# Performance work log

Hardware: AMD Instinct MI355X
Metric: run time of the kernel (lower is better)

## Reference

```python
import jax, jax.numpy as jnp
import numpy as np

L_SPAN = 8          # max event span length
MAX_ITER = 3        # args.max_iteration + 1
RATE = 0.3          # confidence threshold for edge creation
BETA_INTRA = 0.7
BETA_INTER = 0.3


def setup_inputs() -> dict:
    key = jax.random.key(0)
    ks = jax.random.split(key, 16)
    n_sents, S, D = 64, 512, 768
    E, P, NL, H, C = 2000, 20000, 128, 512, 3
    sc = lambda fan: 1.0 / np.sqrt(fan)
    return {
        'sent_emb': jax.random.normal(ks[0], (n_sents, S, D), jnp.float32),
        'W_proj': jax.random.normal(ks[1], (D, NL), jnp.float32) * sc(D),
        'W1': jax.random.normal(ks[2], (2 * D + NL, H), jnp.float32) * sc(2 * D + NL),
        'b1': jnp.zeros((H,), jnp.float32),
        'W2': jax.random.normal(ks[3], (H, C), jnp.float32) * sc(H),
        'b2': jnp.zeros((C,), jnp.float32),
        'W_self': jax.random.normal(ks[4], (NL, NL), jnp.float32) * sc(NL),
        'W_intra': jax.random.normal(ks[5], (NL, NL), jnp.float32) * sc(NL),
        'W_inter': jax.random.normal(ks[6], (NL, NL), jnp.float32) * sc(NL),
        'event_sent': jax.random.randint(ks[7], (E,), 0, n_sents, jnp.int32),
        'event_start': jax.random.randint(ks[8], (E,), 0, S - L_SPAN, jnp.int32),
        'event_len': jax.random.randint(ks[9], (E,), 0, L_SPAN, jnp.int32),
        'pair1': jax.random.randint(ks[10], (P,), 0, E, jnp.int32),
        'pair2': jax.random.randint(ks[11], (P,), 0, E, jnp.int32),
        'rel_type': jax.random.randint(ks[12], (P,), 0, 2, jnp.int32),
        'target': jax.random.randint(ks[13], (P,), 0, 3, jnp.int32),
    }


def _extract_events(sent_emb, event_sent, event_start, event_len):
    # ragged span mean: spans have length 1..L_SPAN
    S = sent_emb.shape[1]
    lens = (event_len + 1).astype(sent_emb.dtype)            # [E]
    offs = jnp.arange(L_SPAN)
    idx = jnp.clip(event_start[:, None] + offs[None, :], 0, S - 1)  # [E, L]
    tok = sent_emb[event_sent[:, None], idx]                 # [E, L, D] gather
    mask = (offs[None, :] < (event_len + 1)[:, None]).astype(sent_emb.dtype)
    return (tok * mask[:, :, None]).sum(1) / lens[:, None]   # [E, D]


def reference(sent_emb, W_proj, W1, b1, W2, b2, W_self, W_intra, W_inter,
              event_sent, event_start, event_len, pair1, pair2, rel_type, target):
    E = event_sent.shape[0]
    e_emb = _extract_events(sent_emb, event_sent, event_start, event_len)   # [E, 768]
    event_pair_embed = jnp.concatenate([e_emb[pair1], e_emb[pair2]], axis=-1)  # [P, 1536]
    x = e_emb @ W_proj                                                      # [E, n_last]

    seg = jax.ops.segment_sum
    loss = jnp.float32(0.0)
    logits = None
    for it in range(MAX_ITER):
        diff = x[pair1] - x[pair2]                                          # [P, n_last]
        feats = jnp.concatenate([event_pair_embed, diff], axis=-1)          # [P, 1536+n_last]
        logits = jax.nn.relu(feats @ W1 + b1) @ W2 + b2                     # [P, C]
        logp = jax.nn.log_softmax(logits, axis=-1)
        ce = -jnp.take_along_axis(logp, target[:, None], axis=-1).mean()
        loss = loss + ce / (it + 1)

        # dynamic graph construction from predictions
        p = jax.nn.softmax(logits, axis=-1)
        conf = p.max(-1) > RATE
        argm = p.argmax(-1)
        f = lambda m: jax.lax.stop_gradient(m.astype(x.dtype))[:, None]
        mi1 = f(conf & (argm == 1) & (rel_type == 0))   # intra: pair1 -> pair2
        mi2 = f(conf & (argm == 2) & (rel_type == 0))   # intra reversed
        me1 = f(conf & (argm == 1) & (rel_type == 1))   # inter
        me2 = f(conf & (argm == 2) & (rel_type == 1))

        # intra aggregation (includes self-loop)
        s_intra = seg(x[pair1] * mi1, pair2, num_segments=E) + \
                  seg(x[pair2] * mi2, pair1, num_segments=E) + x
        c_intra = seg(mi1[:, 0], pair2, num_segments=E) + \
                  seg(mi2[:, 0], pair1, num_segments=E) + 1.0
        agg_intra = s_intra / c_intra[:, None]

        s_inter = seg(x[pair1] * me1, pair2, num_segments=E) + \
                  seg(x[pair2] * me2, pair1, num_segments=E)
        c_inter = seg(me1[:, 0], pair2, num_segments=E) + \
                  seg(me2[:, 0], pair1, num_segments=E)
        agg_inter = s_inter / jnp.maximum(c_inter, 1.0)[:, None]

        x = jax.nn.relu(x @ W_self + BETA_INTRA * (agg_intra @ W_intra)
                        + BETA_INTER * (agg_inter @ W_inter))
    return loss, logits
```

## Files before the change

kernel.cpp:

```cpp
#include <hip/hip_runtime.h>
#include <hip/hip_bf16.h>


#define D_DIM 768
#define H_DIM 512
#define NL_DIM 128

__global__ __launch_bounds__(256) void extract_kernel(
    const float* __restrict__ sent_emb, const int* __restrict__ es,
    const int* __restrict__ st, const int* __restrict__ el,
    float* __restrict__ e_emb)
{
    int e = blockIdx.x;
    int t = threadIdx.x;
    int s = es[e];
    int start = st[e];
    int len = el[e] + 1;
    const float* base = sent_emb + ((size_t)s * 512 + start) * D_DIM;
    float a0 = 0.f, a1 = 0.f, a2 = 0.f;
    for (int k = 0; k < len; ++k) {
        const float* row = base + (size_t)k * D_DIM;
        a0 += row[t];
        a1 += row[t + 256];
        a2 += row[t + 512];
    }
    float inv = 1.0f / (float)len;
    float* out = e_emb + (size_t)e * D_DIM;
    out[t]       = a0 * inv;
    out[t + 256] = a1 * inv;
    out[t + 512] = a2 * inv;
}

#define GBM 64
#define GBN 64
#define GBK 16
__global__ __launch_bounds__(256) void gemm_f32(
    const float* __restrict__ A, int lda,
    const float* __restrict__ B, int ldb,
    float* __restrict__ C, int ldc,
    int M, int N, int K, int flags)
{
    __shared__ float As[GBK][GBM + 4];
    __shared__ float Bs[GBK][GBN];
    int t = threadIdx.x;
    int m0 = blockIdx.y * GBM;
    int n0 = blockIdx.x * GBN;
    int tm = t >> 4;
    int tn = t & 15;
    int arow = t >> 2;
    int akc  = (t & 3) * 4;
    int bkr  = t >> 4;
    int bnc  = (t & 15) * 4;

    float acc[4][4];
#pragma unroll
    for (int i = 0; i < 4; ++i)
#pragma unroll
        for (int j = 0; j < 4; ++j) acc[i][j] = 0.f;

    for (int k0 = 0; k0 < K; k0 += GBK) {
        float4 av = make_float4(0.f, 0.f, 0.f, 0.f);
        if (m0 + arow < M)
            av = *(const float4*)(A + (size_t)(m0 + arow) * lda + k0 + akc);
        As[akc + 0][arow] = av.x;
        As[akc + 1][arow] = av.y;
        As[akc + 2][arow] = av.z;
        As[akc + 3][arow] = av.w;
        float4 bv = *(const float4*)(B + (size_t)(k0 + bkr) * ldb + n0 + bnc);
        *(float4*)&Bs[bkr][bnc] = bv;
        __syncthreads();
#pragma unroll
        for (int k = 0; k < GBK; ++k) {
            float4 a = *(const float4*)&As[k][tm * 4];
            float4 b = *(const float4*)&Bs[k][tn * 4];
            acc[0][0] += a.x * b.x; acc[0][1] += a.x * b.y; acc[0][2] += a.x * b.z; acc[0][3] += a.x * b.w;
            acc[1][0] += a.y * b.x; acc[1][1] += a.y * b.y; acc[1][2] += a.y * b.z; acc[1][3] += a.y * b.w;
            acc[2][0] += a.z * b.x; acc[2][1] += a.z * b.y; acc[2][2] += a.z * b.z; acc[2][3] += a.z * b.w;
            acc[3][0] += a.w * b.x; acc[3][1] += a.w * b.y; acc[3][2] += a.w * b.z; acc[3][3] += a.w * b.w;
        }
        __syncthreads();
    }
#pragma unroll
    for (int i = 0; i < 4; ++i) {
        int row = m0 + tm * 4 + i;
        if (row < M) {
            float* cp = C + (size_t)row * ldc + n0 + tn * 4;
#pragma unroll
            for (int j = 0; j < 4; ++j) {
                float v = acc[i][j];
                if (flags & 1) v += cp[j];
                if (flags & 2) v = fmaxf(v, 0.f);
                cp[j] = v;
            }
        }
    }
}

__global__ __launch_bounds__(256) void zero4_kernel(float4* __restrict__ p, int n4)
{
    int i = blockIdx.x * 256 + threadIdx.x;
    if (i < n4) p[i] = make_float4(0.f, 0.f, 0.f, 0.f);
}

__global__ __launch_bounds__(256) void pair_kernel(
    const float* __restrict__ A1, const float* __restrict__ A2,
    const float* __restrict__ Y, const float* __restrict__ X,
    const float* __restrict__ b1, const float* __restrict__ W2,
    const float* __restrict__ b2,
    const int* __restrict__ pair1, const int* __restrict__ pair2,
    const int* __restrict__ rel, const int* __restrict__ tgt,
    float* s_intra, float* s_inter, float* c_intra, float* c_inter,
    float* __restrict__ ce_out, float* logits_out, int P, int do_scatter)
{
    __shared__ float ce_sh[4];
    int t = threadIdx.x;
    int wave = t >> 6;
    int lane = t & 63;
    int p = blockIdx.x * 4 + wave;
    float ce = 0.f;
    if (p < P) {
        int p1 = pair1[p], p2 = pair2[p];
        int base = lane * 8;
        float a1f[8], a2f[8], y1f[8], y2f[8], b1f[8], w2f[24];
        {
            const float4* a1p = (const float4*)(A1 + (size_t)p1 * H_DIM + base);
            const float4* a2p = (const float4*)(A2 + (size_t)p2 * H_DIM + base);
            const float4* y1p = (const float4*)(Y + (size_t)p1 * H_DIM + base);
            const float4* y2p = (const float4*)(Y + (size_t)p2 * H_DIM + base);
            const float4* b1p = (const float4*)(b1 + base);
            const float4* w2p = (const float4*)(W2 + (size_t)base * 3);
            *(float4*)&a1f[0] = a1p[0]; *(float4*)&a1f[4] = a1p[1];
            *(float4*)&a2f[0] = a2p[0]; *(float4*)&a2f[4] = a2p[1];
            *(float4*)&y1f[0] = y1p[0]; *(float4*)&y1f[4] = y1p[1];
            *(float4*)&y2f[0] = y2p[0]; *(float4*)&y2f[4] = y2p[1];
            *(float4*)&b1f[0] = b1p[0]; *(float4*)&b1f[4] = b1p[1];
#pragma unroll
            for (int q = 0; q < 6; ++q) *(float4*)&w2f[q * 4] = w2p[q];
        }
        float l0 = 0.f, l1 = 0.f, l2 = 0.f;
#pragma unroll
        for (int i = 0; i < 8; ++i) {
            float h = a1f[i] + a2f[i] + y1f[i] - y2f[i] + b1f[i];
            h = fmaxf(h, 0.f);
            l0 += h * w2f[i * 3 + 0];
            l1 += h * w2f[i * 3 + 1];
            l2 += h * w2f[i * 3 + 2];
        }
#pragma unroll
        for (int off = 32; off > 0; off >>= 1) {
            l0 += __shfl_xor(l0, off);
            l1 += __shfl_xor(l1, off);
            l2 += __shfl_xor(l2, off);
        }
        l0 += b2[0]; l1 += b2[1]; l2 += b2[2];
        float m = fmaxf(l0, fmaxf(l1, l2));
        float lse = m + logf(expf(l0 - m) + expf(l1 - m) + expf(l2 - m));
        int tg = tgt[p];
        float lt = (tg == 0) ? l0 : ((tg == 1) ? l1 : l2);
        ce = lse - lt;
        if (logits_out && lane == 0) {
            logits_out[(size_t)p * 3 + 0] = l0;
            logits_out[(size_t)p * 3 + 1] = l1;
            logits_out[(size_t)p * 3 + 2] = l2;
        }
        if (do_scatter) {
            int argm = 0; float mx = l0;
            if (l1 > mx) { mx = l1; argm = 1; }
            if (l2 > mx) { mx = l2; argm = 2; }
            if (argm != 0) {
                int r = rel[p];
                int src = (argm == 1) ? p1 : p2;
                int dst = (argm == 1) ? p2 : p1;
                float* sacc = (r == 0) ? s_intra : s_inter;
                float* cacc = (r == 0) ? c_intra : c_inter;
                const float* xs = X + (size_t)src * NL_DIM;
                float* sd = sacc + (size_t)dst * NL_DIM;
                atomicAdd(&sd[lane], xs[lane]);
                atomicAdd(&sd[lane + 64], xs[lane + 64]);
                if (lane == 0) atomicAdd(&cacc[dst], 1.0f);
            }
        }
    }
    if (lane == 0) ce_sh[wave] = ce;
    __syncthreads();
    if (t == 0) ce_out[blockIdx.x] = ce_sh[0] + ce_sh[1] + ce_sh[2] + ce_sh[3];
}

__global__ __launch_bounds__(256) void agg_kernel(
    const float* __restrict__ s_intra, const float* __restrict__ s_inter,
    const float* __restrict__ c_intra, const float* __restrict__ c_inter,
    const float* __restrict__ X,
    float* __restrict__ aggI, float* __restrict__ aggE, int n)
{
    int i = blockIdx.x * 256 + threadIdx.x;
    if (i >= n) return;
    int e = i >> 7;
    float ci = c_intra[e] + 1.0f;
    float cf = fmaxf(c_inter[e], 1.0f);
    aggI[i] = 0.7f * (s_intra[i] + X[i]) / ci;
    aggE[i] = 0.3f * s_inter[i] / cf;
}

__global__ __launch_bounds__(256) void loss_kernel(
    const float* __restrict__ ce, int nblk, int P, float* __restrict__ out)
{
    int t = threadIdx.x;
    float acc = 0.f;
    for (int it = 0; it < 3; ++it) {
        float w = 1.0f / ((float)P * (float)(it + 1));
        for (int i = t; i < nblk; i += 256)
            acc += ce[(size_t)it * nblk + i] * w;
    }
    __shared__ float red[256];
    red[t] = acc;
    __syncthreads();
    for (int s = 128; s > 0; s >>= 1) {
        if (t < s) red[t] += red[t + s];
        __syncthreads();
    }
    if (t == 0) out[0] = red[0];
}

extern "C" void kernel_launch(void* const* d_in, const int* in_sizes, int n_in,
                              void* d_out, int out_size, void* d_ws, size_t ws_size,
                              hipStream_t stream)
{
    const float* sent_emb  = (const float*)d_in[0];
    const float* W_proj    = (const float*)d_in[1];
    const float* W1        = (const float*)d_in[2];
    const float* b1        = (const float*)d_in[3];
    const float* W2        = (const float*)d_in[4];
    const float* b2        = (const float*)d_in[5];
    const float* W_self    = (const float*)d_in[6];
    const float* W_intra   = (const float*)d_in[7];
    const float* W_inter   = (const float*)d_in[8];
    const int* event_sent  = (const int*)d_in[9];
    const int* event_start = (const int*)d_in[10];
    const int* event_len   = (const int*)d_in[11];
    const int* pair1       = (const int*)d_in[12];
    const int* pair2       = (const int*)d_in[13];
    const int* rel_type    = (const int*)d_in[14];
    const int* target      = (const int*)d_in[15];

    int E = in_sizes[9];
    int P = in_sizes[12];
    float* out = (float*)d_out;
    float* ws  = (float*)d_ws;

    size_t o = 0;
    float* e_emb   = ws + o; o += (size_t)E * D_DIM;
    float* A1      = ws + o; o += (size_t)E * H_DIM;
    float* A2      = ws + o; o += (size_t)E * H_DIM;
    float* Yb      = ws + o; o += (size_t)E * H_DIM;
    float* X0      = ws + o; o += (size_t)E * NL_DIM;
    float* X1      = ws + o; o += (size_t)E * NL_DIM;
    float* s_intra = ws + o; o += (size_t)E * NL_DIM;
    float* s_inter = ws + o; o += (size_t)E * NL_DIM;
    float* c_intra = ws + o; o += (size_t)E;
    float* c_inter = ws + o; o += (size_t)E;
    float* aggI    = ws + o; o += (size_t)E * NL_DIM;
    float* aggE    = ws + o; o += (size_t)E * NL_DIM;
    int NBLK = (P + 3) / 4;
    float* ceb     = ws + o; o += (size_t)3 * NBLK;

    extract_kernel<<<E, 256, 0, stream>>>(sent_emb, event_sent, event_start, event_len, e_emb);

    dim3 gA(H_DIM / GBN, (E + GBM - 1) / GBM);
    dim3 gX(NL_DIM / GBN, (E + GBM - 1) / GBM);
    gemm_f32<<<gA, 256, 0, stream>>>(e_emb, D_DIM, W1, H_DIM, A1, H_DIM, E, H_DIM, D_DIM, 0);
    gemm_f32<<<gA, 256, 0, stream>>>(e_emb, D_DIM, W1 + (size_t)D_DIM * H_DIM, H_DIM, A2, H_DIM, E, H_DIM, D_DIM, 0);
    gemm_f32<<<gX, 256, 0, stream>>>(e_emb, D_DIM, W_proj, NL_DIM, X0, NL_DIM, E, NL_DIM, D_DIM, 0);

    float* xcur = X0;
    float* xnext = X1;
    int zn4 = (E * NL_DIM * 2 + E * 2) / 4;
    for (int it = 0; it < 3; ++it) {
        int last = (it == 2);
        gemm_f32<<<gA, 256, 0, stream>>>(xcur, NL_DIM, W1 + (size_t)2 * D_DIM * H_DIM, H_DIM,
                                         Yb, H_DIM, E, H_DIM, NL_DIM, 0);
        if (!last)
            zero4_kernel<<<(zn4 + 255) / 256, 256, 0, stream>>>((float4*)s_intra, zn4);
        pair_kernel<<<NBLK, 256, 0, stream>>>(A1, A2, Yb, xcur, b1, W2, b2,
                                              pair1, pair2, rel_type, target,
                                              s_intra, s_inter, c_intra, c_inter,
                                              ceb + (size_t)it * NBLK,
                                              last ? (out + 1) : nullptr, P, !last);
        if (!last) {
            agg_kernel<<<(E * NL_DIM + 255) / 256, 256, 0, stream>>>(
                s_intra, s_inter, c_intra, c_inter, xcur, aggI, aggE, E * NL_DIM);
            gemm_f32<<<gX, 256, 0, stream>>>(xcur, NL_DIM, W_self, NL_DIM, xnext, NL_DIM, E, NL_DIM, NL_DIM, 0);
            gemm_f32<<<gX, 256, 0, stream>>>(aggI, NL_DIM, W_intra, NL_DIM, xnext, NL_DIM, E, NL_DIM, NL_DIM, 1);
            gemm_f32<<<gX, 256, 0, stream>>>(aggE, NL_DIM, W_inter, NL_DIM, xnext, NL_DIM, E, NL_DIM, NL_DIM, 1 | 2);
            float* tmp = xcur; xcur = xnext; xnext = tmp;
        }
    }
    loss_kernel<<<1, 256, 0, stream>>>(ceb, NBLK, P, out);
}
```

Baseline: 519.9 us.

## Fold A1/A2/b1 into GEMM epilogue and fuse GEMM launches

The Y GEMM epilogue now builds U = A1 + Y + b1 and V = A2 - Y per event, so the pair kernel gathers two 512-wide rows per pair instead of four and skips the b1 load. The three initial projections become one grid-partitioned launch, and the three update GEMMs become one kernel that accumulates all three products in registers and applies ReLU, with no read-modify-write of the output. The pair kernel handles four pairs per wave with W2 and b2 hoisted out of the pair loop, and span extraction uses float4 loads. The GEMM K-tile grows to 32. This trades some parallelism in the pair kernel and larger shared memory for fewer launches and less gather traffic.

```diff
diff --git a/kernel.cpp b/kernel.cpp
--- a/kernel.cpp
+++ b/kernel.cpp
@@ -5,8 +5,137 @@
 #define D_DIM 768
 #define H_DIM 512
 #define NL_DIM 128
-
-__global__ __launch_bounds__(256) void extract_kernel(
+#define KB 32
+#define TM 64
+#define TN 64
+
+struct Smem {
+    float As[KB][TM + 4];
+    float Bs[KB][TN];
+};
+
+__device__ __forceinline__ void tile_gemm(
+    const float* __restrict__ A, int lda,
+    const float* __restrict__ Bt, int ldb,
+    int m0, int M, int K, Smem& sm, float acc[4][4], int t)
+{
+    int tm = t >> 4, tn = t & 15;
+    for (int k0 = 0; k0 < K; k0 += KB) {
+#pragma unroll
+        for (int r = 0; r < 2; ++r) {
+            int row = (t >> 3) + 32 * r;
+            int c4 = (t & 7) * 4;
+            float4 av = make_float4(0.f, 0.f, 0.f, 0.f);
+            if (m0 + row < M)
+                av = *(const float4*)(A + (size_t)(m0 + row) * lda + k0 + c4);
+            sm.As[c4 + 0][row] = av.x;
+            sm.As[c4 + 1][row] = av.y;
+            sm.As[c4 + 2][row] = av.z;
+            sm.As[c4 + 3][row] = av.w;
+        }
+#pragma unroll
+        for (int r = 0; r < 2; ++r) {
+            int row = (t >> 4) + 16 * r;
+            int c4 = (t & 15) * 4;
+            *(float4*)&sm.Bs[row][c4] =
+                *(const float4*)(Bt + (size_t)(k0 + row) * ldb + c4);
+        }
+        __syncthreads();
+#pragma unroll
+        for (int k = 0; k < KB; ++k) {
+            float4 a = *(const float4*)&sm.As[k][tm * 4];
+            float4 b = *(const float4*)&sm.Bs[k][tn * 4];
+            acc[0][0] += a.x * b.x; acc[0][1] += a.x * b.y; acc[0][2] += a.x * b.z; acc[0][3] += a.x * b.w;
+            acc[1][0] += a.y * b.x; acc[1][1] += a.y * b.y; acc[1][2] += a.y * b.z; acc[1][3] += a.y * b.w;
+            acc[2][0] += a.z * b.x; acc[2][1] += a.z * b.y; acc[2][2] += a.z * b.z; acc[2][3] += a.z * b.w;
+            acc[3][0] += a.w * b.x; acc[3][1] += a.w * b.y; acc[3][2] += a.w * b.z; acc[3][3] += a.w * b.w;
+        }
+        __syncthreads();
+    }
+}
+
+__global__ __launch_bounds__(256) void gemm_a12x0(
+    const float* __restrict__ e_emb, const float* __restrict__ W1,
+    const float* __restrict__ W_proj,
+    float* __restrict__ A1, float* __restrict__ A2, float* __restrict__ X0, int M)
+{
+    __shared__ Smem sm;
+    int t = threadIdx.x;
+    int bx = blockIdx.x;
+    int m0 = blockIdx.y * TM;
+    const float* Bt; float* Ct; int ldb, ldc;
+    if (bx < 8)       { Bt = W1 + bx * 64;                          ldb = 512; Ct = A1 + bx * 64;        ldc = 512; }
+    else if (bx < 16) { Bt = W1 + (size_t)768 * 512 + (bx - 8) * 64; ldb = 512; Ct = A2 + (bx - 8) * 64;  ldc = 512; }
+    else              { Bt = W_proj + (bx - 16) * 64;               ldb = 128; Ct = X0 + (bx - 16) * 64; ldc = 128; }
+    float acc[4][4] = {};
+    tile_gemm(e_emb, D_DIM, Bt, ldb, m0, M, D_DIM, sm, acc, t);
+    int tm = t >> 4, tn = t & 15;
+#pragma unroll
+    for (int i = 0; i < 4; ++i) {
+        int row = m0 + tm * 4 + i;
+        if (row < M)
+            *(float4*)(Ct + (size_t)row * ldc + tn * 4) =
+                make_float4(acc[i][0], acc[i][1], acc[i][2], acc[i][3]);
+    }
+}
+
+__global__ __launch_bounds__(256) void gemm_y_uv(
+    const float* __restrict__ x, const float* __restrict__ W1k,
+    const float* __restrict__ A1, const float* __restrict__ A2,
+    const float* __restrict__ b1,
+    float* __restrict__ U, float* __restrict__ V, int M)
+{
+    __shared__ Smem sm;
+    int t = threadIdx.x;
+    int n0 = blockIdx.x * TN;
+    int m0 = blockIdx.y * TM;
+    float acc[4][4] = {};
+    tile_gemm(x, NL_DIM, W1k + n0, H_DIM, m0, M, NL_DIM, sm, acc, t);
+    int tm = t >> 4, tn = t & 15;
+    float4 b1v = *(const float4*)(b1 + n0 + tn * 4);
+#pragma unroll
+    for (int i = 0; i < 4; ++i) {
+        int row = m0 + tm * 4 + i;
+        if (row < M) {
+            size_t off = (size_t)row * H_DIM + n0 + tn * 4;
+            float4 a1v = *(const float4*)(A1 + off);
+            float4 a2v = *(const float4*)(A2 + off);
+            float4 u, v;
+            u.x = acc[i][0] + a1v.x + b1v.x;  v.x = a2v.x - acc[i][0];
+            u.y = acc[i][1] + a1v.y + b1v.y;  v.y = a2v.y - acc[i][1];
+            u.z = acc[i][2] + a1v.z + b1v.z;  v.z = a2v.z - acc[i][2];
+            u.w = acc[i][3] + a1v.w + b1v.w;  v.w = a2v.w - acc[i][3];
+            *(float4*)(U + off) = u;
+            *(float4*)(V + off) = v;
+        }
+    }
+}
+
+__global__ __launch_bounds__(256) void gemm_update3(
+    const float* __restrict__ x, const float* __restrict__ aggI, const float* __restrict__ aggE,
+    const float* __restrict__ Ws, const float* __restrict__ Wi, const float* __restrict__ We,
+    float* __restrict__ xn, int M)
+{
+    __shared__ Smem sm;
+    int t = threadIdx.x;
+    int n0 = blockIdx.x * TN;
+    int m0 = blockIdx.y * TM;
+    float acc[4][4] = {};
+    tile_gemm(x,    NL_DIM, Ws + n0, NL_DIM, m0, M, NL_DIM, sm, acc, t);
+    tile_gemm(aggI, NL_DIM, Wi + n0, NL_DIM, m0, M, NL_DIM, sm, acc, t);
+    tile_gemm(aggE, NL_DIM, We + n0, NL_DIM, m0, M, NL_DIM, sm, acc, t);
+    int tm = t >> 4, tn = t & 15;
+#pragma unroll
+    for (int i = 0; i < 4; ++i) {
+        int row = m0 + tm * 4 + i;
+        if (row < M)
+            *(float4*)(xn + (size_t)row * NL_DIM + n0 + tn * 4) =
+                make_float4(fmaxf(acc[i][0], 0.f), fmaxf(acc[i][1], 0.f),
+                            fmaxf(acc[i][2], 0.f), fmaxf(acc[i][3], 0.f));
+    }
+}
+
+__global__ __launch_bounds__(192) void extract_kernel(
     const float* __restrict__ sent_emb, const int* __restrict__ es,
     const int* __restrict__ st, const int* __restrict__ el,
     float* __restrict__ e_emb)
@@ -17,83 +146,14 @@
     int start = st[e];
     int len = el[e] + 1;
     const float* base = sent_emb + ((size_t)s * 512 + start) * D_DIM;
-    float a0 = 0.f, a1 = 0.f, a2 = 0.f;
+    float4 a = make_float4(0.f, 0.f, 0.f, 0.f);
     for (int k = 0; k < len; ++k) {
-        const float* row = base + (size_t)k * D_DIM;
-        a0 += row[t];
-        a1 += row[t + 256];
-        a2 += row[t + 512];
+        float4 v = ((const float4*)(base + (size_t)k * D_DIM))[t];
+        a.x += v.x; a.y += v.y; a.z += v.z; a.w += v.w;
     }
     float inv = 1.0f / (float)len;
-    float* out = e_emb + (size_t)e * D_DIM;
-    out[t]       = a0 * inv;
-    out[t + 256] = a1 * inv;
-    out[t + 512] = a2 * inv;
-}
-
-#define GBM 64
-#define GBN 64
-#define GBK 16
-__global__ __launch_bounds__(256) void gemm_f32(
-    const float* __restrict__ A, int lda,
-    const float* __restrict__ B, int ldb,
-    float* __restrict__ C, int ldc,
-    int M, int N, int K, int flags)
-{
-    __shared__ float As[GBK][GBM + 4];
-    __shared__ float Bs[GBK][GBN];
-    int t = threadIdx.x;
-    int m0 = blockIdx.y * GBM;
-    int n0 = blockIdx.x * GBN;
-    int tm = t >> 4;
-    int tn = t & 15;
-    int arow = t >> 2;
-    int akc  = (t & 3) * 4;
-    int bkr  = t >> 4;
-    int bnc  = (t & 15) * 4;
-
-    float acc[4][4];
-#pragma unroll
-    for (int i = 0; i < 4; ++i)
-#pragma unroll
-        for (int j = 0; j < 4; ++j) acc[i][j] = 0.f;
-
-    for (int k0 = 0; k0 < K; k0 += GBK) {
-        float4 av = make_float4(0.f, 0.f, 0.f, 0.f);
-        if (m0 + arow < M)
-            av = *(const float4*)(A + (size_t)(m0 + arow) * lda + k0 + akc);
-        As[akc + 0][arow] = av.x;
-        As[akc + 1][arow] = av.y;
-        As[akc + 2][arow] = av.z;
-        As[akc + 3][arow] = av.w;
-        float4 bv = *(const float4*)(B + (size_t)(k0 + bkr) * ldb + n0 + bnc);
-        *(float4*)&Bs[bkr][bnc] = bv;
-        __syncthreads();
-#pragma unroll
-        for (int k = 0; k < GBK; ++k) {
-            float4 a = *(const float4*)&As[k][tm * 4];
-            float4 b = *(const float4*)&Bs[k][tn * 4];
-            acc[0][0] += a.x * b.x; acc[0][1] += a.x * b.y; acc[0][2] += a.x * b.z; acc[0][3] += a.x * b.w;
-            acc[1][0] += a.y * b.x; acc[1][1] += a.y * b.y; acc[1][2] += a.y * b.z; acc[1][3] += a.y * b.w;
-            acc[2][0] += a.z * b.x; acc[2][1] += a.z * b.y; acc[2][2] += a.z * b.z; acc[2][3] += a.z * b.w;
-            acc[3][0] += a.w * b.x; acc[3][1] += a.w * b.y; acc[3][2] += a.w * b.z; acc[3][3] += a.w * b.w;
-        }
-        __syncthreads();
-    }
-#pragma unroll
-    for (int i = 0; i < 4; ++i) {
-        int row = m0 + tm * 4 + i;
-        if (row < M) {
-            float* cp = C + (size_t)row * ldc + n0 + tn * 4;
-#pragma unroll
-            for (int j = 0; j < 4; ++j) {
-                float v = acc[i][j];
-                if (flags & 1) v += cp[j];
-                if (flags & 2) v = fmaxf(v, 0.f);
-                cp[j] = v;
-            }
-        }
-    }
+    ((float4*)(e_emb + (size_t)e * D_DIM))[t] =
+        make_float4(a.x * inv, a.y * inv, a.z * inv, a.w * inv);
 }
 
 __global__ __launch_bounds__(256) void zero4_kernel(float4* __restrict__ p, int n4)
@@ -103,9 +163,8 @@
 }
 
 __global__ __launch_bounds__(256) void pair_kernel(
-    const float* __restrict__ A1, const float* __restrict__ A2,
-    const float* __restrict__ Y, const float* __restrict__ X,
-    const float* __restrict__ b1, const float* __restrict__ W2,
+    const float* __restrict__ U, const float* __restrict__ V,
+    const float* __restrict__ X, const float* __restrict__ W2,
     const float* __restrict__ b2,
     const int* __restrict__ pair1, const int* __restrict__ pair2,
     const int* __restrict__ rel, const int* __restrict__ tgt,
@@ -116,32 +175,32 @@
     int t = threadIdx.x;
     int wave = t >> 6;
     int lane = t & 63;
-    int p = blockIdx.x * 4 + wave;
+    int base = lane * 8;
+    float w2f[24];
+    {
+        const float4* w2p = (const float4*)(W2 + (size_t)base * 3);
+#pragma unroll
+        for (int q = 0; q < 6; ++q) *(float4*)&w2f[q * 4] = w2p[q];
+    }
+    float b20 = b2[0], b21 = b2[1], b22 = b2[2];
     float ce = 0.f;
-    if (p < P) {
+    int p0 = (blockIdx.x * 4 + wave) * 4;
+#pragma unroll
+    for (int q = 0; q < 4; ++q) {
+        int p = p0 + q;
+        if (p >= P) break;
         int p1 = pair1[p], p2 = pair2[p];
-        int base = lane * 8;
-        float a1f[8], a2f[8], y1f[8], y2f[8], b1f[8], w2f[24];
+        float uf[8], vf[8];
         {
-            const float4* a1p = (const float4*)(A1 + (size_t)p1 * H_DIM + base);
-            const float4* a2p = (const float4*)(A2 + (size_t)p2 * H_DIM + base);
-            const float4* y1p = (const float4*)(Y + (size_t)p1 * H_DIM + base);
-            const float4* y2p = (const float4*)(Y + (size_t)p2 * H_DIM + base);
-            const float4* b1p = (const float4*)(b1 + base);
-            const float4* w2p = (const float4*)(W2 + (size_t)base * 3);
-            *(float4*)&a1f[0] = a1p[0]; *(float4*)&a1f[4] = a1p[1];
-            *(float4*)&a2f[0] = a2p[0]; *(float4*)&a2f[4] = a2p[1];
-            *(float4*)&y1f[0] = y1p[0]; *(float4*)&y1f[4] = y1p[1];
-            *(float4*)&y2f[0] = y2p[0]; *(float4*)&y2f[4] = y2p[1];
-            *(float4*)&b1f[0] = b1p[0]; *(float4*)&b1f[4] = b1p[1];
-#pragma unroll
-            for (int q = 0; q < 6; ++q) *(float4*)&w2f[q * 4] = w2p[q];
+            const float4* up = (const float4*)(U + (size_t)p1 * H_DIM + base);
+            const float4* vp = (const float4*)(V + (size_t)p2 * H_DIM + base);
+            *(float4*)&uf[0] = up[0]; *(float4*)&uf[4] = up[1];
+            *(float4*)&vf[0] = vp[0]; *(float4*)&vf[4] = vp[1];
         }
         float l0 = 0.f, l1 = 0.f, l2 = 0.f;
 #pragma unroll
         for (int i = 0; i < 8; ++i) {
-            float h = a1f[i] + a2f[i] + y1f[i] - y2f[i] + b1f[i];
-            h = fmaxf(h, 0.f);
+            float h = fmaxf(uf[i] + vf[i], 0.f);
             l0 += h * w2f[i * 3 + 0];
             l1 += h * w2f[i * 3 + 1];
             l2 += h * w2f[i * 3 + 2];
@@ -152,12 +211,12 @@
             l1 += __shfl_xor(l1, off);
             l2 += __shfl_xor(l2, off);
         }
-        l0 += b2[0]; l1 += b2[1]; l2 += b2[2];
+        l0 += b20; l1 += b21; l2 += b22;
         float m = fmaxf(l0, fmaxf(l1, l2));
         float lse = m + logf(expf(l0 - m) + expf(l1 - m) + expf(l2 - m));
         int tg = tgt[p];
         float lt = (tg == 0) ? l0 : ((tg == 1) ? l1 : l2);
-        ce = lse - lt;
+        ce += lse - lt;
         if (logits_out && lane == 0) {
             logits_out[(size_t)p * 3 + 0] = l0;
             logits_out[(size_t)p * 3 + 1] = l1;
@@ -251,7 +310,7 @@
     float* e_emb   = ws + o; o += (size_t)E * D_DIM;
     float* A1      = ws + o; o += (size_t)E * H_DIM;
     float* A2      = ws + o; o += (size_t)E * H_DIM;
-    float* Yb      = ws + o; o += (size_t)E * H_DIM;
+    float* V       = ws + o; o += (size_t)E * H_DIM;
     float* X0      = ws + o; o += (size_t)E * NL_DIM;
     float* X1      = ws + o; o += (size_t)E * NL_DIM;
     float* s_intra = ws + o; o += (size_t)E * NL_DIM;
@@ -260,27 +319,27 @@
     float* c_inter = ws + o; o += (size_t)E;
     float* aggI    = ws + o; o += (size_t)E * NL_DIM;
     float* aggE    = ws + o; o += (size_t)E * NL_DIM;
-    int NBLK = (P + 3) / 4;
+    int NBLK = (P + 15) / 16;
     float* ceb     = ws + o; o += (size_t)3 * NBLK;
-
-    extract_kernel<<<E, 256, 0, stream>>>(sent_emb, event_sent, event_start, event_len, e_emb);
-
-    dim3 gA(H_DIM / GBN, (E + GBM - 1) / GBM);
-    dim3 gX(NL_DIM / GBN, (E + GBM - 1) / GBM);
-    gemm_f32<<<gA, 256, 0, stream>>>(e_emb, D_DIM, W1, H_DIM, A1, H_DIM, E, H_DIM, D_DIM, 0);
-    gemm_f32<<<gA, 256, 0, stream>>>(e_emb, D_DIM, W1 + (size_t)D_DIM * H_DIM, H_DIM, A2, H_DIM, E, H_DIM, D_DIM, 0);
-    gemm_f32<<<gX, 256, 0, stream>>>(e_emb, D_DIM, W_proj, NL_DIM, X0, NL_DIM, E, NL_DIM, D_DIM, 0);
-
+    float* U       = e_emb;
+
+    extract_kernel<<<E, 192, 0, stream>>>(sent_emb, event_sent, event_start, event_len, e_emb);
+
+    dim3 gF(18, (E + TM - 1) / TM);
+    gemm_a12x0<<<gF, 256, 0, stream>>>(e_emb, W1, W_proj, A1, A2, X0, E);
+
+    const float* W1k = W1 + (size_t)2 * D_DIM * H_DIM;
+    dim3 gY(H_DIM / TN, (E + TM - 1) / TM);
+    dim3 gU(NL_DIM / TN, (E + TM - 1) / TM);
     float* xcur = X0;
     float* xnext = X1;
     int zn4 = (E * NL_DIM * 2 + E * 2) / 4;
     for (int it = 0; it < 3; ++it) {
         int last = (it == 2);
-        gemm_f32<<<gA, 256, 0, stream>>>(xcur, NL_DIM, W1 + (size_t)2 * D_DIM * H_DIM, H_DIM,
-                                         Yb, H_DIM, E, H_DIM, NL_DIM, 0);
+        gemm_y_uv<<<gY, 256, 0, stream>>>(xcur, W1k, A1, A2, b1, U, V, E);
         if (!last)
             zero4_kernel<<<(zn4 + 255) / 256, 256, 0, stream>>>((float4*)s_intra, zn4);
-        pair_kernel<<<NBLK, 256, 0, stream>>>(A1, A2, Yb, xcur, b1, W2, b2,
+        pair_kernel<<<NBLK, 256, 0, stream>>>(U, V, xcur, W2, b2,
                                               pair1, pair2, rel_type, target,
                                               s_intra, s_inter, c_intra, c_inter,
                                               ceb + (size_t)it * NBLK,
@@ -288,9 +347,7 @@
         if (!last) {
             agg_kernel<<<(E * NL_DIM + 255) / 256, 256, 0, stream>>>(
                 s_intra, s_inter, c_intra, c_inter, xcur, aggI, aggE, E * NL_DIM);
-            gemm_f32<<<gX, 256, 0, stream>>>(xcur, NL_DIM, W_self, NL_DIM, xnext, NL_DIM, E, NL_DIM, NL_DIM, 0);
-            gemm_f32<<<gX, 256, 0, stream>>>(aggI, NL_DIM, W_intra, NL_DIM, xnext, NL_DIM, E, NL_DIM, NL_DIM, 1);
-            gemm_f32<<<gX, 256, 0, stream>>>(aggE, NL_DIM, W_inter, NL_DIM, xnext, NL_DIM, E, NL_DIM, NL_DIM, 1 | 2);
+            gemm_update3<<<gU, 256, 0, stream>>>(xcur, aggI, aggE, W_self, W_intra, W_inter, xnext, E);
             float* tmp = xcur; xcur = xnext; xnext = tmp;
         }
     }
```

Measured after the change: 470.0 us. 1.11x faster.
